# Performance work log

Measured on AMD Instinct MI355X. Metric: run time of the kernel, lower is better.

Reference implementation:

```python
import jax, jax.numpy as jnp
import numpy as np

NUM_GRAPHS = 512


def setup_inputs() -> dict:
    key = jax.random.key(0)
    ks = jax.random.split(key, 12)
    N, E, D, H, C = 100000, 1600000, 128, 128, 10
    x = jax.random.normal(ks[0], (N, D), dtype=jnp.float32)
    edge_index = jax.random.randint(ks[1], (2, E), 0, N, dtype=jnp.int64)
    batch = jnp.sort(jax.random.randint(ks[2], (N,), 0, NUM_GRAPHS, dtype=jnp.int64))
    def glorot(k, fan_in, fan_out):
        s = jnp.sqrt(6.0 / (fan_in + fan_out))
        return jax.random.uniform(k, (fan_in, fan_out), jnp.float32, -s, s)
    return {
        "x": x, "edge_index": edge_index, "batch": batch,
        "W_init": glorot(ks[3], D, H), "b_init": jnp.zeros((H,), jnp.float32),
        "W_h0": glorot(ks[4], H, H), "b_h0": jnp.zeros((H,), jnp.float32),
        "W_h1": glorot(ks[5], H, H), "b_h1": jnp.zeros((H,), jnp.float32),
        "W_out": glorot(ks[6], H, C), "b_out": jnp.zeros((C,), jnp.float32),
    }


def reference(x, edge_index, batch, W_init, b_init, W_h0, b_h0, W_h1, b_h1, W_out, b_out):
    N = x.shape[0]
    loop = jnp.arange(N, dtype=edge_index.dtype)
    # add self-loops (PyG GCNConv default)
    row = jnp.concatenate([edge_index[0], loop])  # source
    col = jnp.concatenate([edge_index[1], loop])  # target
    # symmetric normalization D^-1/2 (A+I) D^-1/2, degrees on target index
    deg = jax.ops.segment_sum(jnp.ones_like(col, dtype=x.dtype), col, num_segments=N)
    dis = jnp.where(deg > 0, jax.lax.rsqrt(jnp.maximum(deg, 1e-12)), 0.0)
    norm = dis[row] * dis[col]  # [E+N]

    def gcn_conv(h, W, b):
        h = h @ W                                    # linear first (as in PyG)
        msg = h[row] * norm[:, None]                 # gather + scale
        return jax.ops.segment_sum(msg, col, num_segments=N) + b  # scatter-add

    h = jax.nn.relu(gcn_conv(x, W_init, b_init))
    h = jax.nn.relu(gcn_conv(h, W_h0, b_h0))
    h = jax.nn.relu(gcn_conv(h, W_h1, b_h1))
    h = gcn_conv(h, W_out, b_out)
    # global mean pooling over graphs
    sums = jax.ops.segment_sum(h, batch, num_segments=NUM_GRAPHS)
    cnt = jax.ops.segment_sum(jnp.ones((N, 1), h.dtype), batch, num_segments=NUM_GRAPHS)
    return sums / jnp.maximum(cnt, 1.0)
```

## Files before the change

### kernel.cpp

```cpp
#include <hip/hip_runtime.h>


#define SCAN_BLOCKS 64
#define SCAN_THREADS (SCAN_BLOCKS * 256)

typedef unsigned short u16;
typedef unsigned int   u32;
typedef __attribute__((ext_vector_type(8))) short bf16x8;
typedef __attribute__((ext_vector_type(4))) float f32x4;

static __device__ __forceinline__ u16 f2bf(float x) {
    u32 u = __float_as_uint(x);
    u32 r = (u + 0x7fffu + ((u >> 16) & 1u)) >> 16;
    return (u16)r;
}
static __device__ __forceinline__ float bf_lo(u32 p) { return __uint_as_float(p << 16); }
static __device__ __forceinline__ float bf_hi(u32 p) { return __uint_as_float(p & 0xffff0000u); }

__global__ __launch_bounds__(256) void k_count(const int* __restrict__ col, int E,
                                               int* __restrict__ cnt,
                                               u16* __restrict__ rank) {
    int e = blockIdx.x * 256 + threadIdx.x;
    if (e < E) rank[e] = (u16)atomicAdd(&cnt[col[e]], 1);
}

__global__ __launch_bounds__(256) void k_scan1(const int* __restrict__ cnt,
                                               int* __restrict__ tsum, int N) {
    int t = blockIdx.x * 256 + threadIdx.x;
    int strip = (N + SCAN_THREADS - 1) / SCAN_THREADS;
    int s0 = t * strip;
    int s1 = s0 + strip; if (s1 > N) s1 = N;
    int s = 0;
    for (int i = s0; i < s1; ++i) s += (cnt[i] + 3) & ~3;
    tsum[t] = s;
}

__global__ __launch_bounds__(1024) void k_scan2(int* __restrict__ tsum) {
    __shared__ int part[1024];
    int t = threadIdx.x;
    int base = t * 16;
    int local[16];
    int s = 0;
    #pragma unroll
    for (int i = 0; i < 16; ++i) { local[i] = tsum[base + i]; s += local[i]; }
    part[t] = s;
    __syncthreads();
    for (int off = 1; off < 1024; off <<= 1) {
        int v = part[t];
        int add = (t >= off) ? part[t - off] : 0;
        __syncthreads();
        part[t] = v + add;
        __syncthreads();
    }
    int run = (t == 0) ? 0 : part[t - 1];
    #pragma unroll
    for (int i = 0; i < 16; ++i) { int c = local[i]; tsum[base + i] = run; run += c; }
}

__global__ __launch_bounds__(256) void k_scan3(const int* __restrict__ cnt,
                                               const int* __restrict__ tsum,
                                               int* __restrict__ rowptr,
                                               float* __restrict__ dis,
                                               int* __restrict__ csr, int N) {
    int t = blockIdx.x * 256 + threadIdx.x;
    int strip = (N + SCAN_THREADS - 1) / SCAN_THREADS;
    int s0 = t * strip;
    int s1 = s0 + strip; if (s1 > N) s1 = N;
    int run = tsum[t];
    for (int i = s0; i < s1; ++i) {
        int c = cnt[i];
        int r = (c + 3) & ~3;
        rowptr[i] = run;
        for (int p = run + c; p < run + r; ++p) csr[p] = N;
        run += r;
        dis[i] = rsqrtf((float)(c + 1));
    }
    if (t == SCAN_THREADS - 1) rowptr[N] = run;
}

__global__ __launch_bounds__(256) void k_fill(const int* __restrict__ row,
                                              const int* __restrict__ col, int E,
                                              const int* __restrict__ rowptr,
                                              const u16* __restrict__ rank,
                                              int* __restrict__ csr) {
    int e = blockIdx.x * 256 + threadIdx.x;
    if (e < E) {
        int c = col[e];
        csr[rowptr[c] + (int)rank[e]] = row[e];
    }
}

__global__ __launch_bounds__(256) void k_cast(const float* __restrict__ src,
                                              const float* __restrict__ dis,
                                              u16* __restrict__ bX,
                                              u16* __restrict__ bA,
                                              u16* __restrict__ bB, int N) {
    int i = blockIdx.x * 256 + threadIdx.x;
    int total = (N + 1) * 32;
    if (i >= total) return;
    int v = i >> 5;
    if (v < N) {
        float dv = dis[v];
        float4 val = ((const float4*)src)[i];
        ushort4 o;
        o.x = f2bf(dv * val.x); o.y = f2bf(dv * val.y);
        o.z = f2bf(dv * val.z); o.w = f2bf(dv * val.w);
        ((ushort4*)bX)[i] = o;
    } else {
        ushort4 z = {0, 0, 0, 0};
        ((ushort4*)bX)[i] = z;
        ((ushort4*)bA)[i] = z;
        ((ushort4*)bB)[i] = z;
    }
}

__global__ __launch_bounds__(256) void k_wprep4(const float* __restrict__ W0,
                                                const float* __restrict__ W1,
                                                const float* __restrict__ W2,
                                                const float* __restrict__ Wo,
                                                u32* __restrict__ whi,
                                                u32* __restrict__ wlo, int C) {
    if (blockIdx.x < 24) {
        int which = blockIdx.x >> 3;
        const float* W = (which == 0) ? W0 : (which == 1) ? W1 : W2;
        int t = (blockIdx.x & 7) * 256 + threadIdx.x;
        int lane = t & 63;
        int nk = t >> 6;
        int k0 = nk & 3;
        int ntile = nk >> 2;
        int n = ntile * 16 + (lane & 15);
        int kbase = k0 * 32 + (lane >> 4) * 8;
        u32 hi[4], lo[4];
        #pragma unroll
        for (int tt = 0; tt < 4; ++tt) {
            float w0 = W[(kbase + 2 * tt) * 128 + n];
            float w1 = W[(kbase + 2 * tt + 1) * 128 + n];
            u16 h0 = f2bf(w0), h1 = f2bf(w1);
            u16 l0 = f2bf(w0 - __uint_as_float((u32)h0 << 16));
            u16 l1 = f2bf(w1 - __uint_as_float((u32)h1 << 16));
            hi[tt] = (u32)h0 | ((u32)h1 << 16);
            lo[tt] = (u32)l0 | ((u32)l1 << 16);
        }
        uint4 qh = {hi[0], hi[1], hi[2], hi[3]};
        uint4 ql = {lo[0], lo[1], lo[2], lo[3]};
        int base = which * 2048;
        ((uint4*)whi)[base + t] = qh;
        ((uint4*)wlo)[base + t] = ql;
    } else {
        int t = threadIdx.x;
        int lane = t & 63;
        int k0 = t >> 6;
        int n = lane & 15;
        int kbase = k0 * 32 + (lane >> 4) * 8;
        bool vc = (n < C);
        u32 hi[4], lo[4];
        #pragma unroll
        for (int tt = 0; tt < 4; ++tt) {
            float w0 = vc ? Wo[(kbase + 2 * tt) * C + n] : 0.f;
            float w1 = vc ? Wo[(kbase + 2 * tt + 1) * C + n] : 0.f;
            u16 h0 = f2bf(w0), h1 = f2bf(w1);
            u16 l0 = f2bf(w0 - __uint_as_float((u32)h0 << 16));
            u16 l1 = f2bf(w1 - __uint_as_float((u32)h1 << 16));
            hi[tt] = (u32)h0 | ((u32)h1 << 16);
            lo[tt] = (u32)l0 | ((u32)l1 << 16);
        }
        uint4 qh = {hi[0], hi[1], hi[2], hi[3]};
        uint4 ql = {lo[0], lo[1], lo[2], lo[3]};
        ((uint4*)whi)[6144 + t] = qh;
        ((uint4*)wlo)[6144 + t] = ql;
    }
}

__global__ __launch_bounds__(256) void k_fused(const u16* __restrict__ hin,
                                               const u32* __restrict__ whi,
                                               const u32* __restrict__ wlo,
                                               const float* __restrict__ bias,
                                               u16* __restrict__ hout,
                                               const int* __restrict__ rowptr,
                                               const int* __restrict__ csr,
                                               const float* __restrict__ dis,
                                               int N, int scale_out,
                                               int proj,
                                               const u32* __restrict__ pwhi,
                                               const u32* __restrict__ pwlo,
                                               u16* __restrict__ tmpC) {
    __shared__ u32 sS[32 * 68];
    __shared__ float dS[32];
    int tid = threadIdx.x;
    int wave = tid >> 6;
    int lane = tid & 63;
    int row0 = blockIdx.x * 32;
    const uint4* hin4 = (const uint4*)hin;

    int grp = lane >> 4;
    int sub = lane & 15;
    #pragma unroll
    for (int jj = 0; jj < 2; ++jj) {
        int rloc = wave * 8 + jj * 4 + grp;
        int row = row0 + rloc;
        bool hR = row < N;
        int ia = 0, rem = 0;
        float dv = 1.f;
        if (hR) {
            ia  = rowptr[row];
            rem = rowptr[row + 1] - ia;
            dv  = dis[row];
        }
        int nself = hR ? row : N;
        uint4 ps = hin4[((u32)nself << 4) + sub];
        float a0 = bf_lo(ps.x), a1 = bf_hi(ps.x);
        float a2 = bf_lo(ps.y), a3 = bf_hi(ps.y);
        float a4 = bf_lo(ps.z), a5 = bf_hi(ps.z);
        float a6 = bf_lo(ps.w), a7 = bf_hi(ps.w);
        int m = rem;
        m = max(m, __shfl_xor(m, 16));
        m = max(m, __shfl_xor(m, 32));
        const int4* cq = (const int4*)(csr + ia);
        for (int k = 0; k < m; k += 8) {
            int4 q0 = cq[(k >> 2)];
            int4 q1 = cq[(k >> 2) + 1];
            bool v0 = k < rem;
            bool v1 = (k + 4) < rem;
            int n0 = v0 ? q0.x : N;
            int n1 = v0 ? q0.y : N;
            int n2 = v0 ? q0.z : N;
            int n3 = v0 ? q0.w : N;
            int n4 = v1 ? q1.x : N;
            int n5 = v1 ? q1.y : N;
            int n6 = v1 ? q1.z : N;
            int n7 = v1 ? q1.w : N;
            uint4 p0 = hin4[((u32)n0 << 4) + sub];
            uint4 p1 = hin4[((u32)n1 << 4) + sub];
            uint4 p2 = hin4[((u32)n2 << 4) + sub];
            uint4 p3 = hin4[((u32)n3 << 4) + sub];
            uint4 p4 = hin4[((u32)n4 << 4) + sub];
            uint4 p5 = hin4[((u32)n5 << 4) + sub];
            uint4 p6 = hin4[((u32)n6 << 4) + sub];
            uint4 p7 = hin4[((u32)n7 << 4) + sub];
            a0 += bf_lo(p0.x) + bf_lo(p1.x) + bf_lo(p2.x) + bf_lo(p3.x);
            a1 += bf_hi(p0.x) + bf_hi(p1.x) + bf_hi(p2.x) + bf_hi(p3.x);
            a2 += bf_lo(p0.y) + bf_lo(p1.y) + bf_lo(p2.y) + bf_lo(p3.y);
            a3 += bf_hi(p0.y) + bf_hi(p1.y) + bf_hi(p2.y) + bf_hi(p3.y);
            a4 += bf_lo(p0.z) + bf_lo(p1.z) + bf_lo(p2.z) + bf_lo(p3.z);
            a5 += bf_hi(p0.z) + bf_hi(p1.z) + bf_hi(p2.z) + bf_hi(p3.z);
            a6 += bf_lo(p0.w) + bf_lo(p1.w) + bf_lo(p2.w) + bf_lo(p3.w);
            a7 += bf_hi(p0.w) + bf_hi(p1.w) + bf_hi(p2.w) + bf_hi(p3.w);
            a0 += bf_lo(p4.x) + bf_lo(p5.x) + bf_lo(p6.x) + bf_lo(p7.x);
            a1 += bf_hi(p4.x) + bf_hi(p5.x) + bf_hi(p6.x) + bf_hi(p7.x);
            a2 += bf_lo(p4.y) + bf_lo(p5.y) + bf_lo(p6.y) + bf_lo(p7.y);
            a3 += bf_hi(p4.y) + bf_hi(p5.y) + bf_hi(p6.y) + bf_hi(p7.y);
            a4 += bf_lo(p4.z) + bf_lo(p5.z) + bf_lo(p6.z) + bf_lo(p7.z);
            a5 += bf_hi(p4.z) + bf_hi(p5.z) + bf_hi(p6.z) + bf_hi(p7.z);
            a6 += bf_lo(p4.w) + bf_lo(p5.w) + bf_lo(p6.w) + bf_lo(p7.w);
            a7 += bf_hi(p4.w) + bf_hi(p5.w) + bf_hi(p6.w) + bf_hi(p7.w);
        }
        u32 w0 = (u32)f2bf(dv * a0) | ((u32)f2bf(dv * a1) << 16);
        u32 w1 = (u32)f2bf(dv * a2) | ((u32)f2bf(dv * a3) << 16);
        u32 w2 = (u32)f2bf(dv * a4) | ((u32)f2bf(dv * a5) << 16);
        u32 w3 = (u32)f2bf(dv * a6) | ((u32)f2bf(dv * a7) << 16);
        sS[rloc * 65 + sub * 4 + 0] = w0;
        sS[rloc * 65 + sub * 4 + 1] = w1;
        sS[rloc * 65 + sub * 4 + 2] = w2;
        sS[rloc * 65 + sub * 4 + 3] = w3;
        if (sub == 0) dS[rloc] = dv;
    }
    __syncthreads();

    f32x4 acc[2][2] = {{{0.f,0.f,0.f,0.f},{0.f,0.f,0.f,0.f}},
                       {{0.f,0.f,0.f,0.f},{0.f,0.f,0.f,0.f}}};
    int mA = lane & 15;
    int qA = lane >> 4;
    #pragma unroll
    for (int k0 = 0; k0 < 4; ++k0) {
        union { u32 u[4]; bf16x8 v; } A0, A1;
        int ub = k0 * 16 + qA * 4;
        #pragma unroll
        for (int tt = 0; tt < 4; ++tt) {
            A0.u[tt] = sS[mA * 65 + ub + tt];
            A1.u[tt] = sS[(mA + 16) * 65 + ub + tt];
        }
        #pragma unroll
        for (int ct = 0; ct < 2; ++ct) {
            int ntk = ((2 * wave + ct) * 4 + k0) * 64 + lane;
            union { uint4 q; bf16x8 v; } BH, BL;
            BH.q = ((const uint4*)whi)[ntk];
            BL.q = ((const uint4*)wlo)[ntk];
            acc[0][ct] = __builtin_amdgcn_mfma_f32_16x16x32_bf16(A0.v, BH.v, acc[0][ct], 0, 0, 0);
            acc[0][ct] = __builtin_amdgcn_mfma_f32_16x16x32_bf16(A0.v, BL.v, acc[0][ct], 0, 0, 0);
            acc[1][ct] = __builtin_amdgcn_mfma_f32_16x16x32_bf16(A1.v, BH.v, acc[1][ct], 0, 0, 0);
            acc[1][ct] = __builtin_amdgcn_mfma_f32_16x16x32_bf16(A1.v, BL.v, acc[1][ct], 0, 0, 0);
        }
    }

    if (!proj) {
        #pragma unroll
        for (int rt = 0; rt < 2; ++rt) {
            #pragma unroll
            for (int ct = 0; ct < 2; ++ct) {
                int col = (2 * wave + ct) * 16 + (lane & 15);
                float bb = bias[col];
                #pragma unroll
                for (int r = 0; r < 4; ++r) {
                    int rloc = rt * 16 + (lane >> 4) * 4 + r;
                    int row = row0 + rloc;
                    if (row < N) {
                        float o = fmaxf(acc[rt][ct][r] + bb, 0.f);
                        if (scale_out) o *= dS[rloc];
                        hout[((u32)row << 7) + col] = f2bf(o);
                    }
                }
            }
        }
    } else {
        __syncthreads();
        u16* hS16 = (u16*)sS;
        #pragma unroll
        for (int rt = 0; rt < 2; ++rt) {
            #pragma unroll
            for (int ct = 0; ct < 2; ++ct) {
                int col = (2 * wave + ct) * 16 + (lane & 15);
                float bb = bias[col];
                #pragma unroll
                for (int r = 0; r < 4; ++r) {
                    int rloc = rt * 16 + (lane >> 4) * 4 + r;
                    hS16[rloc * 136 + col] = f2bf(fmaxf(acc[rt][ct][r] + bb, 0.f));
                }
            }
        }
        __syncthreads();
        if (wave < 2) {
            int m2 = lane & 15;
            int quad = lane >> 4;
            f32x4 a2 = {0.f, 0.f, 0.f, 0.f};
            #pragma unroll
            for (int k0 = 0; k0 < 4; ++k0) {
                bf16x8 Afrag = *(bf16x8*)&hS16[(wave * 16 + m2) * 136 + k0 * 32 + quad * 8];
                union { uint4 q; bf16x8 v; } BH, BL;
                BH.q = ((const uint4*)pwhi)[k0 * 64 + lane];
                BL.q = ((const uint4*)pwlo)[k0 * 64 + lane];
                a2 = __builtin_amdgcn_mfma_f32_16x16x32_bf16(Afrag, BH.v, a2, 0, 0, 0);
                a2 = __builtin_amdgcn_mfma_f32_16x16x32_bf16(Afrag, BL.v, a2, 0, 0, 0);
            }
            #pragma unroll
            for (int r = 0; r < 4; ++r) {
                int rloc = wave * 16 + quad * 4 + r;
                int row = row0 + rloc;
                if (row < N) tmpC[((u32)row << 4) + m2] = f2bf(a2[r] * dS[rloc]);
            }
        }
        if (blockIdx.x == 0 && tid < 16) tmpC[((u32)N << 4) + tid] = 0;
    }
}

__global__ __launch_bounds__(1024) void k_aggpool(const u16* __restrict__ tp,
                                                  const int* __restrict__ rowptr,
                                                  const int* __restrict__ csr,
                                                  const float* __restrict__ dis,
                                                  const int* __restrict__ batch,
                                                  const float* __restrict__ bout,
                                                  float* __restrict__ out,
                                                  int N, int C) {
    __shared__ float2 red[1024];
    int g = blockIdx.x;
    int tid = threadIdx.x;
    int c = tid & 7;
    int rg = tid >> 3;
    const u32* tp32 = (const u32*)tp;
    int lo = 0, hi = N;
    while (lo < hi) { int m = (lo + hi) >> 1; if (batch[m] < g) lo = m + 1; else hi = m; }
    int lb = lo;
    hi = N;
    while (lo < hi) { int m = (lo + hi) >> 1; if (batch[m] <= g) lo = m + 1; else hi = m; }
    int ub = lo;
    const int4* csr4 = (const int4*)csr;
    float px = 0.f, py = 0.f;
    for (int v = lb + rg; v < ub; v += 128) {
        u32 ps = tp32[((u32)v << 3) + c];
        float ax = bf_lo(ps), ay = bf_hi(ps);
        int i = rowptr[v], e = rowptr[v + 1];
        for (; i + 8 <= e; i += 8) {
            int4 q0 = csr4[(u32)i >> 2];
            int4 q1 = csr4[((u32)i >> 2) + 1];
            u32 p0 = tp32[((u32)q0.x << 3) + c];
            u32 p1 = tp32[((u32)q0.y << 3) + c];
            u32 p2 = tp32[((u32)q0.z << 3) + c];
            u32 p3 = tp32[((u32)q0.w << 3) + c];
            u32 p4 = tp32[((u32)q1.x << 3) + c];
            u32 p5 = tp32[((u32)q1.y << 3) + c];
            u32 p6 = tp32[((u32)q1.z << 3) + c];
            u32 p7 = tp32[((u32)q1.w << 3) + c];
            ax += bf_lo(p0) + bf_lo(p1) + bf_lo(p2) + bf_lo(p3)
                + bf_lo(p4) + bf_lo(p5) + bf_lo(p6) + bf_lo(p7);
            ay += bf_hi(p0) + bf_hi(p1) + bf_hi(p2) + bf_hi(p3)
                + bf_hi(p4) + bf_hi(p5) + bf_hi(p6) + bf_hi(p7);
        }
        if (i < e) {
            int4 q0 = csr4[(u32)i >> 2];
            u32 p0 = tp32[((u32)q0.x << 3) + c];
            u32 p1 = tp32[((u32)q0.y << 3) + c];
            u32 p2 = tp32[((u32)q0.z << 3) + c];
            u32 p3 = tp32[((u32)q0.w << 3) + c];
            ax += bf_lo(p0) + bf_lo(p1) + bf_lo(p2) + bf_lo(p3);
            ay += bf_hi(p0) + bf_hi(p1) + bf_hi(p2) + bf_hi(p3);
        }
        float dv = dis[v];
        px += dv * ax;
        py += dv * ay;
    }
    red[tid] = make_float2(px, py);
    __syncthreads();
    #pragma unroll
    for (int s = 64; s >= 1; s >>= 1) {
        if (rg < s) {
            float2 o = red[tid + s * 8];
            red[tid].x += o.x; red[tid].y += o.y;
        }
        __syncthreads();
    }
    if (tid < 8) {
        float cnt = (float)(ub - lb);
        float den = fmaxf(cnt, 1.0f);
        float2 s2 = red[tid];
        int ch0 = 2 * tid, ch1 = 2 * tid + 1;
        if (ch0 < C) out[g * C + ch0] = (s2.x + cnt * bout[ch0]) / den;
        if (ch1 < C) out[g * C + ch1] = (s2.y + cnt * bout[ch1]) / den;
    }
}

extern "C" void kernel_launch(void* const* d_in, const int* in_sizes, int n_in,
                              void* d_out, int out_size, void* d_ws, size_t ws_size,
                              hipStream_t stream) {
    const float* x      = (const float*)d_in[0];
    const int*   ei     = (const int*)d_in[1];
    const int*   batch  = (const int*)d_in[2];
    const float* W_init = (const float*)d_in[3];
    const float* b_init = (const float*)d_in[4];
    const float* W_h0   = (const float*)d_in[5];
    const float* b_h0   = (const float*)d_in[6];
    const float* W_h1   = (const float*)d_in[7];
    const float* b_h1   = (const float*)d_in[8];
    const float* W_out  = (const float*)d_in[9];
    const float* b_out  = (const float*)d_in[10];

    int N = in_sizes[0] / 128;
    int E = in_sizes[1] / 2;
    int C = in_sizes[10];
    int G = out_size / C;

    size_t off = 0;
    auto alloc = [&](size_t bytes) -> char* {
        char* p = (char*)d_ws + off;
        off += (bytes + 255) & ~(size_t)255;
        return p;
    };
    u16*   bufX   = (u16*)  alloc((size_t)(N + 1) * 128 * 2);
    u16*   bufA   = (u16*)  alloc((size_t)(N + 1) * 128 * 2);
    u16*   bufB   = (u16*)  alloc((size_t)(N + 1) * 128 * 2);
    float* dis    = (float*)alloc((size_t)N * 4);
    int*   rowptr = (int*)  alloc((size_t)(N + 1) * 4);
    int*   csr    = (int*)  alloc(((size_t)E + 3 * (size_t)N + 8) * 4);
    int*   tsum   = (int*)  alloc((size_t)SCAN_THREADS * 4);
    u32*   whi    = (u32*)  alloc((3 * 2048 + 256) * 16);
    u32*   wlo    = (u32*)  alloc((3 * 2048 + 256) * 16);
    size_t zoff   = off;
    int*   cnt    = (int*)  alloc((size_t)N * 4);
    size_t zbytes = off - zoff;

    u16*   rank   = (u16*)bufB;
    u16*   tmpC   = (u16*)bufX;

    hipMemsetAsync(cnt, 0, zbytes, stream);

    const int* rowi = ei;
    const int* coli = ei + E;

    int eb = (E + 255) / 256;
    k_count<<<eb, 256, 0, stream>>>(coli, E, cnt, rank);
    k_scan1<<<SCAN_BLOCKS, 256, 0, stream>>>(cnt, tsum, N);
    k_scan2<<<1, 1024, 0, stream>>>(tsum);
    k_scan3<<<SCAN_BLOCKS, 256, 0, stream>>>(cnt, tsum, rowptr, dis, csr, N);
    k_fill<<<eb, 256, 0, stream>>>(rowi, coli, E, rowptr, rank, csr);

    k_wprep4<<<25, 256, 0, stream>>>(W_init, W_h0, W_h1, W_out, whi, wlo, C);

    int cg = ((N + 1) * 32 + 255) / 256;
    k_cast<<<cg, 256, 0, stream>>>(x, dis, bufX, bufA, bufB, N);

    int fb = (N + 31) / 32;

    k_fused<<<fb, 256, 0, stream>>>(bufX, whi,         wlo,         b_init, bufA, rowptr, csr, dis, N, 1, 0, nullptr, nullptr, nullptr);
    k_fused<<<fb, 256, 0, stream>>>(bufA, whi + 8192,  wlo + 8192,  b_h0,   bufB, rowptr, csr, dis, N, 1, 0, nullptr, nullptr, nullptr);
    k_fused<<<fb, 256, 0, stream>>>(bufB, whi + 16384, wlo + 16384, b_h1,   bufA, rowptr, csr, dis, N, 0, 1, whi + 24576, wlo + 24576, tmpC);

    k_aggpool<<<G, 1024, 0, stream>>>(tmpC, rowptr, csr, dis, batch, b_out, (float*)d_out, N, C);
}
```

Before: 438.3 us.

## Sort nodes by in-degree to balance aggregation work within waves and blocks

Adds a counting sort of nodes by in-degree (histogram, bin prefix, scatter) and builds the CSR in that permuted order. The fused layer kernel walks nodes in permuted order, so the 4 rows sharing a wave have similar degree and waste fewer iterations on the max-degree loop. Blocks are also launched in reverse so the high-degree tiles start first. Costs several extra small kernels, perm/iperm indirection and scattered output writes. Row ordering from atomics is nondeterministic but the result does not depend on it.

```diff
diff --git a/kernel.cpp b/kernel.cpp
--- a/kernel.cpp
+++ b/kernel.cpp
@@ -24,14 +24,55 @@
     if (e < E) rank[e] = (u16)atomicAdd(&cnt[col[e]], 1);
 }
 
-__global__ __launch_bounds__(256) void k_scan1(const int* __restrict__ cnt,
+__global__ __launch_bounds__(256) void k_hist(const int* __restrict__ cnt, int N,
+                                              int* __restrict__ histo) {
+    int i = blockIdx.x * 256 + threadIdx.x;
+    if (i < N) atomicAdd(&histo[min(cnt[i], 255)], 1);
+}
+
+__global__ __launch_bounds__(256) void k_binpfx(const int* __restrict__ histo,
+                                                int* __restrict__ binbase) {
+    __shared__ int s[256];
+    int t = threadIdx.x;
+    s[t] = histo[t];
+    __syncthreads();
+    for (int off = 1; off < 256; off <<= 1) {
+        int v = s[t];
+        int a = (t >= off) ? s[t - off] : 0;
+        __syncthreads();
+        s[t] = v + a;
+        __syncthreads();
+    }
+    binbase[t] = (t == 0) ? 0 : s[t - 1];
+}
+
+__global__ __launch_bounds__(256) void k_scatter(const int* __restrict__ cnt, int N,
+                                                 int* __restrict__ binbase,
+                                                 int* __restrict__ perm,
+                                                 int* __restrict__ iperm,
+                                                 int* __restrict__ slotpos,
+                                                 int* __restrict__ cdeg,
+                                                 float* __restrict__ dis) {
+    int i = blockIdx.x * 256 + threadIdx.x;
+    if (i >= N) return;
+    int c = cnt[i];
+    int b = min(c, 255);
+    int pos = atomicAdd(&binbase[b], 1);
+    perm[pos] = i;
+    iperm[i] = pos;
+    slotpos[pos] = (c + 3) & ~3;
+    cdeg[pos] = c;
+    dis[i] = rsqrtf((float)(c + 1));
+}
+
+__global__ __launch_bounds__(256) void k_scan1(const int* __restrict__ slotpos,
                                                int* __restrict__ tsum, int N) {
     int t = blockIdx.x * 256 + threadIdx.x;
     int strip = (N + SCAN_THREADS - 1) / SCAN_THREADS;
     int s0 = t * strip;
     int s1 = s0 + strip; if (s1 > N) s1 = N;
     int s = 0;
-    for (int i = s0; i < s1; ++i) s += (cnt[i] + 3) & ~3;
+    for (int i = s0; i < s1; ++i) s += slotpos[i];
     tsum[t] = s;
 }
 
@@ -57,10 +98,10 @@
     for (int i = 0; i < 16; ++i) { int c = local[i]; tsum[base + i] = run; run += c; }
 }
 
-__global__ __launch_bounds__(256) void k_scan3(const int* __restrict__ cnt,
+__global__ __launch_bounds__(256) void k_scan3(const int* __restrict__ slotpos,
+                                               const int* __restrict__ cdeg,
                                                const int* __restrict__ tsum,
                                                int* __restrict__ rowptr,
-                                               float* __restrict__ dis,
                                                int* __restrict__ csr, int N) {
     int t = blockIdx.x * 256 + threadIdx.x;
     int strip = (N + SCAN_THREADS - 1) / SCAN_THREADS;
@@ -68,12 +109,11 @@
     int s1 = s0 + strip; if (s1 > N) s1 = N;
     int run = tsum[t];
     for (int i = s0; i < s1; ++i) {
-        int c = cnt[i];
-        int r = (c + 3) & ~3;
         rowptr[i] = run;
+        int c = cdeg[i];
+        int r = slotpos[i];
         for (int p = run + c; p < run + r; ++p) csr[p] = N;
         run += r;
-        dis[i] = rsqrtf((float)(c + 1));
     }
     if (t == SCAN_THREADS - 1) rowptr[N] = run;
 }
@@ -81,12 +121,13 @@
 __global__ __launch_bounds__(256) void k_fill(const int* __restrict__ row,
                                               const int* __restrict__ col, int E,
                                               const int* __restrict__ rowptr,
+                                              const int* __restrict__ iperm,
                                               const u16* __restrict__ rank,
                                               int* __restrict__ csr) {
     int e = blockIdx.x * 256 + threadIdx.x;
     if (e < E) {
         int c = col[e];
-        csr[rowptr[c] + (int)rank[e]] = row[e];
+        csr[rowptr[iperm[c]] + (int)rank[e]] = row[e];
     }
 }
 
@@ -179,6 +220,7 @@
                                                const int* __restrict__ rowptr,
                                                const int* __restrict__ csr,
                                                const float* __restrict__ dis,
+                                               const int* __restrict__ perm,
                                                int N, int scale_out,
                                                int proj,
                                                const u32* __restrict__ pwhi,
@@ -186,10 +228,11 @@
                                                u16* __restrict__ tmpC) {
     __shared__ u32 sS[32 * 68];
     __shared__ float dS[32];
+    __shared__ int pS[32];
     int tid = threadIdx.x;
     int wave = tid >> 6;
     int lane = tid & 63;
-    int row0 = blockIdx.x * 32;
+    int row0 = ((int)gridDim.x - 1 - (int)blockIdx.x) * 32;
     const uint4* hin4 = (const uint4*)hin;
 
     int grp = lane >> 4;
@@ -197,17 +240,17 @@
     #pragma unroll
     for (int jj = 0; jj < 2; ++jj) {
         int rloc = wave * 8 + jj * 4 + grp;
-        int row = row0 + rloc;
-        bool hR = row < N;
-        int ia = 0, rem = 0;
+        int p = row0 + rloc;
+        bool hR = p < N;
+        int ia = 0, rem = 0, r = N;
         float dv = 1.f;
         if (hR) {
-            ia  = rowptr[row];
-            rem = rowptr[row + 1] - ia;
-            dv  = dis[row];
-        }
-        int nself = hR ? row : N;
-        uint4 ps = hin4[((u32)nself << 4) + sub];
+            r   = perm[p];
+            ia  = rowptr[p];
+            rem = rowptr[p + 1] - ia;
+            dv  = dis[r];
+        }
+        uint4 ps = hin4[((u32)r << 4) + sub];
         float a0 = bf_lo(ps.x), a1 = bf_hi(ps.x);
         float a2 = bf_lo(ps.y), a3 = bf_hi(ps.y);
         float a4 = bf_lo(ps.z), a5 = bf_hi(ps.z);
@@ -262,7 +305,7 @@
         sS[rloc * 65 + sub * 4 + 1] = w1;
         sS[rloc * 65 + sub * 4 + 2] = w2;
         sS[rloc * 65 + sub * 4 + 3] = w3;
-        if (sub == 0) dS[rloc] = dv;
+        if (sub == 0) { dS[rloc] = dv; pS[rloc] = r; }
     }
     __syncthreads();
 
@@ -302,11 +345,11 @@
                 #pragma unroll
                 for (int r = 0; r < 4; ++r) {
                     int rloc = rt * 16 + (lane >> 4) * 4 + r;
-                    int row = row0 + rloc;
-                    if (row < N) {
+                    if (row0 + rloc < N) {
+                        int rr = pS[rloc];
                         float o = fmaxf(acc[rt][ct][r] + bb, 0.f);
                         if (scale_out) o *= dS[rloc];
-                        hout[((u32)row << 7) + col] = f2bf(o);
+                        hout[((u32)rr << 7) + col] = f2bf(o);
                     }
                 }
             }
@@ -344,8 +387,10 @@
             #pragma unroll
             for (int r = 0; r < 4; ++r) {
                 int rloc = wave * 16 + quad * 4 + r;
-                int row = row0 + rloc;
-                if (row < N) tmpC[((u32)row << 4) + m2] = f2bf(a2[r] * dS[rloc]);
+                if (row0 + rloc < N) {
+                    int rr = pS[rloc];
+                    tmpC[((u32)rr << 4) + m2] = f2bf(a2[r] * dS[rloc]);
+                }
             }
         }
         if (blockIdx.x == 0 && tid < 16) tmpC[((u32)N << 4) + tid] = 0;
@@ -355,6 +400,7 @@
 __global__ __launch_bounds__(1024) void k_aggpool(const u16* __restrict__ tp,
                                                   const int* __restrict__ rowptr,
                                                   const int* __restrict__ csr,
+                                                  const int* __restrict__ iperm,
                                                   const float* __restrict__ dis,
                                                   const int* __restrict__ batch,
                                                   const float* __restrict__ bout,
@@ -377,7 +423,8 @@
     for (int v = lb + rg; v < ub; v += 128) {
         u32 ps = tp32[((u32)v << 3) + c];
         float ax = bf_lo(ps), ay = bf_hi(ps);
-        int i = rowptr[v], e = rowptr[v + 1];
+        int pos = iperm[v];
+        int i = rowptr[pos], e = rowptr[pos + 1];
         for (; i + 8 <= e; i += 8) {
             int4 q0 = csr4[(u32)i >> 2];
             int4 q1 = csr4[((u32)i >> 2) + 1];
@@ -462,8 +509,14 @@
     int*   tsum   = (int*)  alloc((size_t)SCAN_THREADS * 4);
     u32*   whi    = (u32*)  alloc((3 * 2048 + 256) * 16);
     u32*   wlo    = (u32*)  alloc((3 * 2048 + 256) * 16);
+    int*   perm   = (int*)  alloc((size_t)N * 4);
+    int*   iperm  = (int*)  alloc((size_t)N * 4);
+    int*   slotpos= (int*)  alloc((size_t)N * 4);
+    int*   cdeg   = (int*)  alloc((size_t)N * 4);
+    int*   binbase= (int*)  alloc(256 * 4);
     size_t zoff   = off;
     int*   cnt    = (int*)  alloc((size_t)N * 4);
+    int*   histo  = (int*)  alloc(256 * 4);
     size_t zbytes = off - zoff;
 
     u16*   rank   = (u16*)bufB;
@@ -475,11 +528,15 @@
     const int* coli = ei + E;
 
     int eb = (E + 255) / 256;
+    int nb = (N + 255) / 256;
     k_count<<<eb, 256, 0, stream>>>(coli, E, cnt, rank);
-    k_scan1<<<SCAN_BLOCKS, 256, 0, stream>>>(cnt, tsum, N);
+    k_hist<<<nb, 256, 0, stream>>>(cnt, N, histo);
+    k_binpfx<<<1, 256, 0, stream>>>(histo, binbase);
+    k_scatter<<<nb, 256, 0, stream>>>(cnt, N, binbase, perm, iperm, slotpos, cdeg, dis);
+    k_scan1<<<SCAN_BLOCKS, 256, 0, stream>>>(slotpos, tsum, N);
     k_scan2<<<1, 1024, 0, stream>>>(tsum);
-    k_scan3<<<SCAN_BLOCKS, 256, 0, stream>>>(cnt, tsum, rowptr, dis, csr, N);
-    k_fill<<<eb, 256, 0, stream>>>(rowi, coli, E, rowptr, rank, csr);
+    k_scan3<<<SCAN_BLOCKS, 256, 0, stream>>>(slotpos, cdeg, tsum, rowptr, csr, N);
+    k_fill<<<eb, 256, 0, stream>>>(rowi, coli, E, rowptr, iperm, rank, csr);
 
     k_wprep4<<<25, 256, 0, stream>>>(W_init, W_h0, W_h1, W_out, whi, wlo, C);
 
@@ -488,9 +545,9 @@
 
     int fb = (N + 31) / 32;
 
-    k_fused<<<fb, 256, 0, stream>>>(bufX, whi,         wlo,         b_init, bufA, rowptr, csr, dis, N, 1, 0, nullptr, nullptr, nullptr);
-    k_fused<<<fb, 256, 0, stream>>>(bufA, whi + 8192,  wlo + 8192,  b_h0,   bufB, rowptr, csr, dis, N, 1, 0, nullptr, nullptr, nullptr);
-    k_fused<<<fb, 256, 0, stream>>>(bufB, whi + 16384, wlo + 16384, b_h1,   bufA, rowptr, csr, dis, N, 0, 1, whi + 24576, wlo + 24576, tmpC);
-
-    k_aggpool<<<G, 1024, 0, stream>>>(tmpC, rowptr, csr, dis, batch, b_out, (float*)d_out, N, C);
-}
+    k_fused<<<fb, 256, 0, stream>>>(bufX, whi,         wlo,         b_init, bufA, rowptr, csr, dis, perm, N, 1, 0, nullptr, nullptr, nullptr);
+    k_fused<<<fb, 256, 0, stream>>>(bufA, whi + 8192,  wlo + 8192,  b_h0,   bufB, rowptr, csr, dis, perm, N, 1, 0, nullptr, nullptr, nullptr);
+    k_fused<<<fb, 256, 0, stream>>>(bufB, whi + 16384, wlo + 16384, b_h1,   bufA, rowptr, csr, dis, perm, N, 0, 1, whi + 24576, wlo + 24576, tmpC);
+
+    k_aggpool<<<G, 1024, 0, stream>>>(tmpC, rowptr, csr, iperm, dis, batch, b_out, (float*)d_out, N, C);
+}
```

After: 970.6 us. 2.21x slower.
